# Performance work log

Hardware: AMD Instinct MI355X
Metric: run time of the kernel (lower is better)

## Reference

```python
import jax, jax.numpy as jnp
import numpy as np

B, N, V, X, H, C = 128, 1023, 32000, 256, 256, 10  # N = 2^10 - 1 perfect binary tree (heap layout)


def setup_inputs() -> dict:
    key = jax.random.key(0)
    ks = jax.random.split(key, 12)
    s = 0.02
    return {
        "wordid": jax.random.randint(ks[0], (B, N), 0, V),
        "h0": jnp.zeros((B, N, H), jnp.float32),
        "c0": jnp.zeros((B, N, H), jnp.float32),
        "emb": jax.random.normal(ks[1], (V, X), jnp.float32) * s,
        "W_iou": jax.random.normal(ks[2], (3 * H, X), jnp.float32) * s,
        "U_iou": jax.random.normal(ks[3], (3 * H, 2 * H), jnp.float32) * s,
        "b_iou": jnp.zeros((1, 3 * H), jnp.float32),
        "Uf_W": jax.random.normal(ks[4], (2 * H, 2 * H), jnp.float32) * s,
        "Uf_b": jnp.zeros((2 * H,), jnp.float32),
        "Wmem": jax.random.normal(ks[5], (H, H), jnp.float32) * s,
        "wh_W": jax.random.normal(ks[6], (H, H), jnp.float32) * s,
        "wh_b": jnp.zeros((H,), jnp.float32),
        "lin_W": jax.random.normal(ks[7], (C, H), jnp.float32) * s,
        "lin_b": jnp.zeros((C,), jnp.float32),
    }


def _apply_node(iou, b_iou, c_in):
    # TreeLSTMCell.apply_node_func: iou -> i,o,u gates; c = sig(i)*tanh(u) + c_in; h = sig(o)*tanh(c)
    i, o, u = jnp.split(iou + b_iou, 3, axis=-1)
    c = jax.nn.sigmoid(i) * jnp.tanh(u) + c_in
    h = jax.nn.sigmoid(o) * jnp.tanh(c)
    return h, c


def reference(wordid, h0, c0, emb, W_iou, U_iou, b_iou, Uf_W, Uf_b, Wmem, wh_W, wh_b, lin_W, lin_b):
    Bn, Nn, Hn = h0.shape
    D = int(np.log2(Nn + 1))  # depth of perfect binary tree
    h, c = h0, c0
    # --- leaves (frontier 0): iou = W_iou(embed), c from initial state ---
    s = 2 ** (D - 1) - 1
    x_leaf = emb[wordid[:, s:]]                                  # [B, Nleaf, X]
    iou = jnp.einsum('bnx,gx->bng', x_leaf, W_iou)               # [B, Nleaf, 3H]
    hl, cl = _apply_node(iou, b_iou, c[:, s:])
    h = h.at[:, s:].set(hl)
    c = c.at[:, s:].set(cl)
    # --- internal levels, bottom-up (reduce_func overwrites iou and c) ---
    for level in range(D - 2, -1, -1):
        ps, pe = 2 ** level - 1, 2 ** (level + 1) - 1
        npar = pe - ps
        cs, ce = pe, pe + 2 * npar  # children of parent p live at 2p+1, 2p+2 (contiguous block)
        h_cat = h[:, cs:ce].reshape(Bn, npar, 2 * Hn)            # [B, npar, 2H]
        f = jax.nn.sigmoid(jnp.einsum('bnk,jk->bnj', h_cat, Uf_W) + Uf_b)
        f = f.reshape(Bn, npar, 2, Hn)
        c_sum = jnp.sum(f * c[:, cs:ce].reshape(Bn, npar, 2, Hn), axis=2)
        iou_p = jnp.einsum('bnk,gk->bng', h_cat, U_iou)          # [B, npar, 3H]
        hp, cp = _apply_node(iou_p, b_iou, c_sum)
        h = h.at[:, ps:pe].set(hp)
        c = c.at[:, ps:pe].set(cp)
    # --- TreeAttention: root (node 0 per tree) attends over all nodes of its tree ---
    dec = h[:, 0]                                                # [B, H]
    proj = jnp.einsum('bnh,gh->bng', h, Wmem)                    # memory_project
    scores = jnp.einsum('bh,bnh->bn', dec, proj)
    attn = jax.nn.softmax(scores, axis=1)                        # MaskedSoftmax, mask=None
    context = jnp.einsum('bn,bnh->bh', attn, h)                  # [B, H]
    hid = jax.nn.relu(context @ wh_W.T + wh_b)
    return hid @ lin_W.T + lin_b                                 # [B, num_classes]
```

## Files before the change

### kernel.cpp

```cpp
#include <hip/hip_runtime.h>
#include <math.h>

#define BB      128
#define NNODES  1023
#define HD      256
#define LEAVES  512
#define IOU3    768
#define CAT2    512
#define LDCOMB  1280

typedef unsigned short ushort_t;
typedef __bf16 bf16x8 __attribute__((ext_vector_type(8)));
typedef float  f32x4  __attribute__((ext_vector_type(4)));

__device__ __forceinline__ float sigf(float x) { return 1.0f / (1.0f + expf(-x)); }

__device__ __forceinline__ void gload16(const void* g, void* l)
{
    __builtin_amdgcn_global_load_lds(
        (const __attribute__((address_space(1))) unsigned int*)g,
        (__attribute__((address_space(3))) unsigned int*)l, 16, 0, 0);
}

__device__ __forceinline__ void split_bf16(float x, ushort_t& h, ushort_t& l)
{
    unsigned u = __float_as_uint(x);
    unsigned r = u + 0x7fff + ((u >> 16) & 1);
    h = (ushort_t)(r >> 16);
    float fh = __uint_as_float((unsigned)h << 16);
    float d = x - fh;
    unsigned u2 = __float_as_uint(d);
    unsigned r2 = u2 + 0x7fff + ((u2 >> 16) & 1);
    l = (ushort_t)(r2 >> 16);
}

__device__ __forceinline__ void split4v(float4 v, ushort4& hv, ushort4& lv)
{
    split_bf16(v.x, hv.x, lv.x);
    split_bf16(v.y, hv.y, lv.y);
    split_bf16(v.z, hv.z, lv.z);
    split_bf16(v.w, hv.w, lv.w);
}

__device__ __forceinline__ float rh2(ushort_t h, ushort_t l)
{
    return __uint_as_float((unsigned)h << 16) + __uint_as_float((unsigned)l << 16);
}

__global__ void k_splits(const float* __restrict__ emb, const float* __restrict__ W_iou,
                         const float* __restrict__ Uf, const float* __restrict__ Ui,
                         ushort_t* __restrict__ ehi, ushort_t* __restrict__ elo,
                         ushort_t* __restrict__ wihi, ushort_t* __restrict__ wilo,
                         ushort_t* __restrict__ wchi, ushort_t* __restrict__ wclo,
                         int V)
{
    const int stride = gridDim.x * 256;
    const int t0 = blockIdx.x * 256 + threadIdx.x;
    ushort4 hv, lv;
    for (int i = t0; i < V * 64; i += stride) {
        split4v(((const float4*)emb)[i], hv, lv);
        ((ushort4*)ehi)[i] = hv;
        ((ushort4*)elo)[i] = lv;
    }
    for (int i = t0; i < IOU3 * 64; i += stride) {
        split4v(((const float4*)W_iou)[i], hv, lv);
        ((ushort4*)wihi)[i] = hv;
        ((ushort4*)wilo)[i] = lv;
    }
    for (int i = t0; i < 1280 * 128; i += stride) {
        int row = i >> 7, c4 = i & 127;
        const float* src = (row < 512) ? (Uf + (size_t)row * 512)
                                       : (Ui + (size_t)(row - 512) * 512);
        split4v(((const float4*)src)[c4], hv, lv);
        ((ushort4*)wchi)[i] = hv;
        ((ushort4*)wclo)[i] = lv;
    }
}

#define BM 128
#define BN 128
#define BK 32

__global__ __launch_bounds__(512, 4)
void gemm_mfma(const ushort_t* __restrict__ Ahi, const ushort_t* __restrict__ Alo,
               int lognpar, unsigned sB, int sP, int m0, int K,
               const ushort_t* __restrict__ Bhi, const ushort_t* __restrict__ Blo,
               float* __restrict__ C, int ldc)
{
    __shared__ __align__(16) char lds[65536];
    const int tid = threadIdx.x;

    int bx = blockIdx.x, by = blockIdx.y;
    {
        const int gx = gridDim.x, gy = gridDim.y;
        if ((gx & 7) == 0) {
            int f = by * gx + bx;
            int span = gy << 3;
            int s = f / span;
            int wv = f - s * span;
            bx = (s << 3) + (wv & 7);
            by = wv >> 3;
        }
    }

    const int w = tid >> 6, lane = tid & 63;

    unsigned aoff, boff;
    {
        int row = tid >> 2;
        int slotp = (tid & 3) ^ ((row >> 1) & 3);
        int mg = m0 + bx * BM + row;
        int b = mg >> lognpar;
        int q = mg & ((1 << lognpar) - 1);
        unsigned ab = (unsigned)b * sB + (unsigned)q * (unsigned)sP;
        aoff = ab + slotp * 8;
        boff = (unsigned)(by * BN + row) * (unsigned)K + slotp * 8;
    }
    const int wdst = w * 1024;

    auto STAGE = [&](int k0, char* buf) {
        gload16(Ahi + aoff + k0, buf +     0 + wdst);
        gload16(Alo + aoff + k0, buf +  8192 + wdst);
        gload16(Bhi + boff + k0, buf + 16384 + wdst);
        gload16(Blo + boff + k0, buf + 24576 + wdst);
    };

    const int wm = w >> 2, wn = w & 3;
    const int rA0 = wm * 64 + (lane & 15);
    const int rB0 = wn * 32 + (lane & 15);
    const int ko = lane >> 4;
    const int rdA = rA0 * 64 + ((ko ^ ((rA0 >> 1) & 3)) << 4);
    const int rdB = rB0 * 64 + ((ko ^ ((rB0 >> 1) & 3)) << 4);

    f32x4 acc[4][2];
#pragma unroll
    for (int mi = 0; mi < 4; ++mi)
#pragma unroll
        for (int ni = 0; ni < 2; ++ni) acc[mi][ni] = (f32x4){0.f, 0.f, 0.f, 0.f};

    const int nt = K / BK;
    STAGE(0, lds);
    int cur = 0;
    for (int t = 0; t < nt; ++t) {
        if (t + 1 < nt) {
            STAGE((t + 1) * BK, lds + (cur ^ 1) * 32768);
            asm volatile("s_waitcnt vmcnt(4)" ::: "memory");
        } else {
            asm volatile("s_waitcnt vmcnt(0)" ::: "memory");
        }
        __builtin_amdgcn_s_barrier();
        __builtin_amdgcn_sched_barrier(0);
        char* base = lds + cur * 32768;
        bf16x8 ah[4], al[4], bh[2], bl[2];
#pragma unroll
        for (int q = 0; q < 4; ++q) {
            ah[q] = *(const bf16x8*)(base +        rdA + q * 1024);
            al[q] = *(const bf16x8*)(base + 8192 + rdA + q * 1024);
        }
#pragma unroll
        for (int q = 0; q < 2; ++q) {
            bh[q] = *(const bf16x8*)(base + 16384 + rdB + q * 1024);
            bl[q] = *(const bf16x8*)(base + 24576 + rdB + q * 1024);
        }
        __builtin_amdgcn_s_setprio(1);
#pragma unroll
        for (int mi = 0; mi < 4; ++mi)
#pragma unroll
            for (int ni = 0; ni < 2; ++ni) {
                acc[mi][ni] = __builtin_amdgcn_mfma_f32_16x16x32_bf16(ah[mi], bh[ni], acc[mi][ni], 0, 0, 0);
                acc[mi][ni] = __builtin_amdgcn_mfma_f32_16x16x32_bf16(ah[mi], bl[ni], acc[mi][ni], 0, 0, 0);
                acc[mi][ni] = __builtin_amdgcn_mfma_f32_16x16x32_bf16(al[mi], bh[ni], acc[mi][ni], 0, 0, 0);
            }
        __builtin_amdgcn_s_setprio(0);
        __builtin_amdgcn_s_barrier();
        cur ^= 1;
    }

    {
        char* patch = lds + w * 2304;
        const int cl = lane & 15, rg = lane >> 4;
        const int gcol0 = by * BN + wn * 32;
#pragma unroll
        for (int mi = 0; mi < 4; ++mi) {
#pragma unroll
            for (int ni = 0; ni < 2; ++ni)
#pragma unroll
                for (int r = 0; r < 4; ++r)
                    *(float*)(patch + (rg * 4 + r) * 144 + (ni * 16 + cl) * 4) = acc[mi][ni][r];
            int grow0 = m0 + bx * BM + wm * 64 + mi * 16;
#pragma unroll
            for (int i = 0; i < 2; ++i) {
                int slot = lane + 64 * i;
                int lr = slot >> 3, c4 = slot & 7;
                f32x4 vv = *(const f32x4*)(patch + lr * 144 + c4 * 16);
                *(f32x4*)(C + (size_t)(grow0 + lr) * ldc + gcol0 + c4 * 4) = vv;
            }
        }
    }
}

__global__ void k_apply_leaf(const float* __restrict__ viou, const int* __restrict__ wordid,
                             const float* __restrict__ b_iou,
                             ushort_t* __restrict__ hhi, ushort_t* __restrict__ hlo,
                             float* __restrict__ c)
{
    int idx = blockIdx.x * 256 + threadIdx.x;
    int m_l = idx >> 8, hh = idx & 255;
    int b = m_l >> 9, leaf = m_l & 511;
    int node = 511 + leaf;
    int word = wordid[b * NNODES + node];
    const float* br = viou + (size_t)word * IOU3;
    float iv = br[hh]        + b_iou[hh];
    float ov = br[256 + hh]  + b_iou[256 + hh];
    float uv = br[512 + hh]  + b_iou[512 + hh];
    size_t nb = ((size_t)b * NNODES + node) * HD + hh;
    float cn = sigf(iv) * tanhf(uv);
    float hn = sigf(ov) * tanhf(cn);
    c[nb] = cn;
    split_bf16(hn, hhi[nb], hlo[nb]);
}

__global__ void k_apply_level(const float* __restrict__ buf, const float* __restrict__ b_iou,
                              const float* __restrict__ Uf_b,
                              ushort_t* __restrict__ hhi, ushort_t* __restrict__ hlo,
                              float* __restrict__ c,
                              int lognpar, int ps, int cs)
{
    int idx = blockIdx.x * 256 + threadIdx.x;
    int m_l = idx >> 8, hh = idx & 255;
    int b = m_l >> lognpar;
    int p = m_l & ((1 << lognpar) - 1);
    const float* br = buf + (size_t)m_l * LDCOMB;
    float fl = sigf(br[hh]        + Uf_b[hh]);
    float fr = sigf(br[256 + hh]  + Uf_b[256 + hh]);
    size_t cb = ((size_t)b * NNODES + cs + 2 * p) * HD + hh;
    float csum = fl * c[cb] + fr * c[cb + HD];
    float iv = br[512 + hh]  + b_iou[hh];
    float ov = br[768 + hh]  + b_iou[256 + hh];
    float uv = br[1024 + hh] + b_iou[512 + hh];
    float cn = sigf(iv) * tanhf(uv) + csum;
    float hn = sigf(ov) * tanhf(cn);
    size_t pb = ((size_t)b * NNODES + ps + p) * HD + hh;
    c[pb] = cn;
    split_bf16(hn, hhi[pb], hlo[pb]);
}

__global__ void k_dec_v(const ushort_t* __restrict__ hhi, const ushort_t* __restrict__ hlo,
                        const float* __restrict__ Wmem, float* __restrict__ v)
{
    int b = blockIdx.x, k = threadIdx.x;
    __shared__ float dec[HD];
    size_t base = (size_t)b * NNODES * HD;
    dec[k] = rh2(hhi[base + k], hlo[base + k]);
    __syncthreads();
    float s = 0.f;
    for (int g = 0; g < HD; ++g) s = fmaf(dec[g], Wmem[g * HD + k], s);
    v[b * HD + k] = s;
}

__global__ void k_scores(const ushort_t* __restrict__ hhi, const ushort_t* __restrict__ hlo,
                         const float* __restrict__ v, float* __restrict__ scores)
{
    int b = blockIdx.x;
    int w = threadIdx.x >> 6, lane = threadIdx.x & 63;
    int n = blockIdx.y * 4 + w;
    if (n >= NNODES) return;
    size_t hb = ((size_t)b * NNODES + n) * HD;
    ushort4 ph = *(const ushort4*)(hhi + hb + lane * 4);
    ushort4 pl = *(const ushort4*)(hlo + hb + lane * 4);
    float4 vv = *(const float4*)(v + b * HD + lane * 4);
    float s = rh2(ph.x, pl.x) * vv.x + rh2(ph.y, pl.y) * vv.y +
              rh2(ph.z, pl.z) * vv.z + rh2(ph.w, pl.w) * vv.w;
#pragma unroll
    for (int o = 32; o; o >>= 1) s += __shfl_down(s, o);
    if (lane == 0) scores[(size_t)b * NNODES + n] = s;
}

__global__ void k_context(const ushort_t* __restrict__ hhi, const ushort_t* __restrict__ hlo,
                          const float* __restrict__ scores, float* __restrict__ partial)
{
    int b = blockIdx.x, ch = blockIdx.y, k = threadIdx.x;
    __shared__ float red[4];
    __shared__ float wts[128];
    const float* srow = scores + (size_t)b * NNODES;

    float sv[4];
    float m = -INFINITY;
#pragma unroll
    for (int i = 0; i < 4; ++i) {
        int n = k + 256 * i;
        sv[i] = (n < NNODES) ? srow[n] : -INFINITY;
        m = fmaxf(m, sv[i]);
    }
#pragma unroll
    for (int o = 32; o; o >>= 1) m = fmaxf(m, __shfl_xor(m, o));
    int w = k >> 6, lane = k & 63;
    if (lane == 0) red[w] = m;
    __syncthreads();
    m = fmaxf(fmaxf(red[0], red[1]), fmaxf(red[2], red[3]));
    __syncthreads();
    float s = 0.f;
#pragma unroll
    for (int i = 0; i < 4; ++i) {
        int n = k + 256 * i;
        s += (n < NNODES) ? expf(sv[i] - m) : 0.f;
    }
#pragma unroll
    for (int o = 32; o; o >>= 1) s += __shfl_xor(s, o);
    if (lane == 0) red[w] = s;
    __syncthreads();
    float inv = 1.0f / (red[0] + red[1] + red[2] + red[3]);

    int n0 = ch * 128;
    if (k < 128) {
        int n = n0 + k;
        wts[k] = (n < NNODES) ? expf(srow[n] - m) * inv : 0.f;
    }
    __syncthreads();

    int n1 = n0 + 128; if (n1 > NNODES) n1 = NNODES;
    float acc = 0.f;
    for (int n = n0; n < n1; ++n) {
        size_t i = ((size_t)b * NNODES + n) * HD + k;
        acc = fmaf(wts[n - n0], rh2(hhi[i], hlo[i]), acc);
    }
    partial[((size_t)b * 8 + ch) * HD + k] = acc;
}

__global__ void k_final(const float* __restrict__ partial,
                        const float* __restrict__ wh_W, const float* __restrict__ wh_b,
                        const float* __restrict__ lin_W, const float* __restrict__ lin_b,
                        float* __restrict__ out)
{
    int b = blockIdx.x, j = threadIdx.x;
    __shared__ float ctx[HD];
    __shared__ float hid[HD];
    float s = 0.f;
#pragma unroll
    for (int ch = 0; ch < 8; ++ch) s += partial[((size_t)b * 8 + ch) * HD + j];
    ctx[j] = s;
    __syncthreads();
    float a = wh_b[j];
    for (int k = 0; k < HD; ++k) a = fmaf(ctx[k], wh_W[j * HD + k], a);
    hid[j] = fmaxf(a, 0.f);
    __syncthreads();
    if (j < 10) {
        float o = lin_b[j];
        for (int k = 0; k < HD; ++k) o = fmaf(hid[k], lin_W[j * HD + k], o);
        out[b * 10 + j] = o;
    }
}

extern "C" void kernel_launch(void* const* d_in, const int* in_sizes, int n_in,
                              void* d_out, int out_size, void* d_ws, size_t ws_size,
                              hipStream_t stream)
{
    const int*   wordid = (const int*)d_in[0];
    const float* emb    = (const float*)d_in[3];
    const float* W_iou  = (const float*)d_in[4];
    const float* U_iou  = (const float*)d_in[5];
    const float* b_iou  = (const float*)d_in[6];
    const float* Uf_W   = (const float*)d_in[7];
    const float* Uf_b   = (const float*)d_in[8];
    const float* Wmem   = (const float*)d_in[9];
    const float* wh_W   = (const float*)d_in[10];
    const float* wh_b   = (const float*)d_in[11];
    const float* lin_W  = (const float*)d_in[12];
    const float* lin_b  = (const float*)d_in[13];
    float* out = (float*)d_out;

    const int V = in_sizes[3] / 256;
    const size_t nh = (size_t)BB * NNODES * HD;

    char* ws = (char*)d_ws;
    size_t off = 0;
    auto alloc = [&](size_t bytes) -> void* {
        void* p = ws + off;
        off += (bytes + 255) & ~(size_t)255;
        return p;
    };
    ushort_t* hhi  = (ushort_t*)alloc(nh * 2);
    ushort_t* hlo  = (ushort_t*)alloc(nh * 2);
    float*    c    = (float*)   alloc(nh * 4);
    ushort_t* ehi  = (ushort_t*)alloc((size_t)V * 256 * 2);
    ushort_t* elo  = (ushort_t*)alloc((size_t)V * 256 * 2);
    ushort_t* wchi = (ushort_t*)alloc((size_t)LDCOMB * 512 * 2);
    ushort_t* wclo = (ushort_t*)alloc((size_t)LDCOMB * 512 * 2);
    ushort_t* wihi = (ushort_t*)alloc((size_t)IOU3 * 256 * 2);
    ushort_t* wilo = (ushort_t*)alloc((size_t)IOU3 * 256 * 2);
    float* v       = (float*)alloc((size_t)BB * HD * 4);
    float* scores  = (float*)alloc((size_t)BB * NNODES * 4);
    float* partial = (float*)alloc((size_t)BB * 8 * HD * 4);
    float* buf     = (float*)alloc((size_t)32768 * LDCOMB * 4);
    float* viou    = buf;
    (void)ws_size;

    k_splits<<<2048, 256, 0, stream>>>(emb, W_iou, Uf_W, U_iou,
                                       ehi, elo, wihi, wilo, wchi, wclo, V);

    {
        dim3 g(256, 6);
        gemm_mfma<<<g, 512, 0, stream>>>(ehi, elo, 0, 256u, 0, 0, 256,
                                         wihi, wilo, viou, IOU3);
        k_apply_leaf<<<65536, 256, 0, stream>>>(viou, wordid, b_iou, hhi, hlo, c);
    }

    for (int L = 8; L >= 0; --L) {
        int npar = 1 << L;
        int ps = npar - 1, cs = 2 * npar - 1;
        const ushort_t* Abh = hhi + (size_t)cs * HD;
        const ushort_t* Abl = hlo + (size_t)cs * HD;
        dim3 g(npar, 10);
        gemm_mfma<<<g, 512, 0, stream>>>(Abh, Abl, L,
                                         (unsigned)(NNODES * HD), 2 * HD, 0, CAT2,
                                         wchi, wclo, buf, LDCOMB);
        k_apply_level<<<BB * npar, 256, 0, stream>>>(buf, b_iou, Uf_b, hhi, hlo, c,
                                                     L, ps, cs);
    }

    k_dec_v<<<BB, HD, 0, stream>>>(hhi, hlo, Wmem, v);
    k_scores<<<dim3(BB, 256), 256, 0, stream>>>(hhi, hlo, v, scores);
    k_context<<<dim3(BB, 8), HD, 0, stream>>>(hhi, hlo, scores, partial);
    k_final<<<BB, HD, 0, stream>>>(partial, wh_W, wh_b, lin_W, lin_b, out);
}
```

Baseline: 666.9 us.

## Fuse forget-gate GEMM with per-level cell update epilogue

Splits the combined per-level GEMM into an iou GEMM that writes a narrower buffer and a new forget-gate GEMM kernel, gemm_f. gemm_f's epilogue computes the sigmoid gates, child-c sum, the cell and hidden update, and the bf16 split directly from its accumulators. Uf rows are permuted so each block's tile holds matching left and right gate columns for the same hidden indices. This removes the separate apply kernel and the write and reread of the forget-gate part of the intermediate buffer. In exchange the epilogue does scattered loads of c and ioubuf straight from global memory instead of through LDS.

```diff
diff --git a/kernel.cpp b/kernel.cpp
--- a/kernel.cpp
+++ b/kernel.cpp
@@ -7,7 +7,6 @@
 #define LEAVES  512
 #define IOU3    768
 #define CAT2    512
-#define LDCOMB  1280
 
 typedef unsigned short ushort_t;
 typedef __bf16 bf16x8 __attribute__((ext_vector_type(8)));
@@ -51,7 +50,8 @@
                          const float* __restrict__ Uf, const float* __restrict__ Ui,
                          ushort_t* __restrict__ ehi, ushort_t* __restrict__ elo,
                          ushort_t* __restrict__ wihi, ushort_t* __restrict__ wilo,
-                         ushort_t* __restrict__ wchi, ushort_t* __restrict__ wclo,
+                         ushort_t* __restrict__ uihi, ushort_t* __restrict__ uilo,
+                         ushort_t* __restrict__ wfhi, ushort_t* __restrict__ wflo,
                          int V)
 {
     const int stride = gridDim.x * 256;
@@ -67,13 +67,19 @@
         ((ushort4*)wihi)[i] = hv;
         ((ushort4*)wilo)[i] = lv;
     }
-    for (int i = t0; i < 1280 * 128; i += stride) {
-        int row = i >> 7, c4 = i & 127;
-        const float* src = (row < 512) ? (Uf + (size_t)row * 512)
-                                       : (Ui + (size_t)(row - 512) * 512);
+    for (int i = t0; i < IOU3 * 128; i += stride) {
+        split4v(((const float4*)Ui)[i], hv, lv);
+        ((ushort4*)uihi)[i] = hv;
+        ((ushort4*)uilo)[i] = lv;
+    }
+    for (int i = t0; i < 512 * 128; i += stride) {
+        int rowp = i >> 7, c4 = i & 127;
+        int hb = rowp >> 5, rem = rowp & 31;
+        int g = rem >> 4, hl = rem & 15;
+        const float* src = Uf + (size_t)(g * 256 + hb * 16 + hl) * 512;
         split4v(((const float4*)src)[c4], hv, lv);
-        ((ushort4*)wchi)[i] = hv;
-        ((ushort4*)wclo)[i] = lv;
+        ((ushort4*)wfhi)[i] = hv;
+        ((ushort4*)wflo)[i] = lv;
     }
 }
 
@@ -194,6 +200,134 @@
                 int lr = slot >> 3, c4 = slot & 7;
                 f32x4 vv = *(const f32x4*)(patch + lr * 144 + c4 * 16);
                 *(f32x4*)(C + (size_t)(grow0 + lr) * ldc + gcol0 + c4 * 4) = vv;
+            }
+        }
+    }
+}
+
+__global__ __launch_bounds__(512, 4)
+void gemm_f(const ushort_t* __restrict__ Ahi, const ushort_t* __restrict__ Alo,
+            int L, unsigned sB, int sP,
+            const ushort_t* __restrict__ Bhi, const ushort_t* __restrict__ Blo,
+            const float* __restrict__ ioubuf, const float* __restrict__ Uf_b,
+            const float* __restrict__ b_iou,
+            float* __restrict__ c, ushort_t* __restrict__ hhi, ushort_t* __restrict__ hlo,
+            int ps, int cs)
+{
+    __shared__ __align__(16) char lds[65536];
+    const int tid = threadIdx.x;
+    const int K = 512;
+
+    int bx = blockIdx.x, by = blockIdx.y;
+    {
+        const int gx = gridDim.x, gy = gridDim.y;
+        if ((gx & 7) == 0) {
+            int f = by * gx + bx;
+            int span = gy << 3;
+            int s = f / span;
+            int wv = f - s * span;
+            bx = (s << 3) + (wv & 7);
+            by = wv >> 3;
+        }
+    }
+
+    const int w = tid >> 6, lane = tid & 63;
+
+    unsigned aoff, boff;
+    {
+        int row = tid >> 2;
+        int slotp = (tid & 3) ^ ((row >> 1) & 3);
+        int mg = bx * BM + row;
+        int b = mg >> L;
+        int q = mg & ((1 << L) - 1);
+        unsigned ab = (unsigned)b * sB + (unsigned)q * (unsigned)sP;
+        aoff = ab + slotp * 8;
+        boff = (unsigned)(by * BN + row) * (unsigned)K + slotp * 8;
+    }
+    const int wdst = w * 1024;
+
+    auto STAGE = [&](int k0, char* buf) {
+        gload16(Ahi + aoff + k0, buf +     0 + wdst);
+        gload16(Alo + aoff + k0, buf +  8192 + wdst);
+        gload16(Bhi + boff + k0, buf + 16384 + wdst);
+        gload16(Blo + boff + k0, buf + 24576 + wdst);
+    };
+
+    const int wm = w >> 2, wn = w & 3;
+    const int rA0 = wm * 64 + (lane & 15);
+    const int rB0 = wn * 32 + (lane & 15);
+    const int ko = lane >> 4;
+    const int rdA = rA0 * 64 + ((ko ^ ((rA0 >> 1) & 3)) << 4);
+    const int rdB = rB0 * 64 + ((ko ^ ((rB0 >> 1) & 3)) << 4);
+
+    f32x4 acc[4][2];
+#pragma unroll
+    for (int mi = 0; mi < 4; ++mi)
+#pragma unroll
+        for (int ni = 0; ni < 2; ++ni) acc[mi][ni] = (f32x4){0.f, 0.f, 0.f, 0.f};
+
+    const int nt = K / BK;
+    STAGE(0, lds);
+    int cur = 0;
+    for (int t = 0; t < nt; ++t) {
+        if (t + 1 < nt) {
+            STAGE((t + 1) * BK, lds + (cur ^ 1) * 32768);
+            asm volatile("s_waitcnt vmcnt(4)" ::: "memory");
+        } else {
+            asm volatile("s_waitcnt vmcnt(0)" ::: "memory");
+        }
+        __builtin_amdgcn_s_barrier();
+        __builtin_amdgcn_sched_barrier(0);
+        char* base = lds + cur * 32768;
+        bf16x8 ah[4], al[4], bh[2], bl[2];
+#pragma unroll
+        for (int q = 0; q < 4; ++q) {
+            ah[q] = *(const bf16x8*)(base +        rdA + q * 1024);
+            al[q] = *(const bf16x8*)(base + 8192 + rdA + q * 1024);
+        }
+#pragma unroll
+        for (int q = 0; q < 2; ++q) {
+            bh[q] = *(const bf16x8*)(base + 16384 + rdB + q * 1024);
+            bl[q] = *(const bf16x8*)(base + 24576 + rdB + q * 1024);
+        }
+        __builtin_amdgcn_s_setprio(1);
+#pragma unroll
+        for (int mi = 0; mi < 4; ++mi)
+#pragma unroll
+            for (int ni = 0; ni < 2; ++ni) {
+                acc[mi][ni] = __builtin_amdgcn_mfma_f32_16x16x32_bf16(ah[mi], bh[ni], acc[mi][ni], 0, 0, 0);
+                acc[mi][ni] = __builtin_amdgcn_mfma_f32_16x16x32_bf16(ah[mi], bl[ni], acc[mi][ni], 0, 0, 0);
+                acc[mi][ni] = __builtin_amdgcn_mfma_f32_16x16x32_bf16(al[mi], bh[ni], acc[mi][ni], 0, 0, 0);
+            }
+        __builtin_amdgcn_s_setprio(0);
+        __builtin_amdgcn_s_barrier();
+        cur ^= 1;
+    }
+
+    {
+        const int hh = by * 64 + wn * 16 + (lane & 15);
+        const int npm1 = (1 << L) - 1;
+#pragma unroll
+        for (int mi = 0; mi < 4; ++mi) {
+            int grow0 = bx * BM + wm * 64 + mi * 16 + (lane >> 4) * 4;
+#pragma unroll
+            for (int r = 0; r < 4; ++r) {
+                int grow = grow0 + r;
+                float fl = sigf(acc[mi][0][r] + Uf_b[hh]);
+                float fr = sigf(acc[mi][1][r] + Uf_b[256 + hh]);
+                int b = grow >> L;
+                int p = grow & npm1;
+                size_t cb = ((size_t)b * NNODES + cs + 2 * p) * HD + hh;
+                float csum = fl * c[cb] + fr * c[cb + HD];
+                size_t iob = (size_t)grow * IOU3 + hh;
+                float iv = ioubuf[iob]       + b_iou[hh];
+                float ov = ioubuf[iob + 256] + b_iou[256 + hh];
+                float uv = ioubuf[iob + 512] + b_iou[512 + hh];
+                float cn = sigf(iv) * tanhf(uv) + csum;
+                float hn = sigf(ov) * tanhf(cn);
+                size_t pb = ((size_t)b * NNODES + ps + p) * HD + hh;
+                c[pb] = cn;
+                split_bf16(hn, hhi[pb], hlo[pb]);
             }
         }
     }
@@ -220,31 +354,6 @@
     split_bf16(hn, hhi[nb], hlo[nb]);
 }
 
-__global__ void k_apply_level(const float* __restrict__ buf, const float* __restrict__ b_iou,
-                              const float* __restrict__ Uf_b,
-                              ushort_t* __restrict__ hhi, ushort_t* __restrict__ hlo,
-                              float* __restrict__ c,
-                              int lognpar, int ps, int cs)
-{
-    int idx = blockIdx.x * 256 + threadIdx.x;
-    int m_l = idx >> 8, hh = idx & 255;
-    int b = m_l >> lognpar;
-    int p = m_l & ((1 << lognpar) - 1);
-    const float* br = buf + (size_t)m_l * LDCOMB;
-    float fl = sigf(br[hh]        + Uf_b[hh]);
-    float fr = sigf(br[256 + hh]  + Uf_b[256 + hh]);
-    size_t cb = ((size_t)b * NNODES + cs + 2 * p) * HD + hh;
-    float csum = fl * c[cb] + fr * c[cb + HD];
-    float iv = br[512 + hh]  + b_iou[hh];
-    float ov = br[768 + hh]  + b_iou[256 + hh];
-    float uv = br[1024 + hh] + b_iou[512 + hh];
-    float cn = sigf(iv) * tanhf(uv) + csum;
-    float hn = sigf(ov) * tanhf(cn);
-    size_t pb = ((size_t)b * NNODES + ps + p) * HD + hh;
-    c[pb] = cn;
-    split_bf16(hn, hhi[pb], hlo[pb]);
-}
-
 __global__ void k_dec_v(const ushort_t* __restrict__ hhi, const ushort_t* __restrict__ hlo,
                         const float* __restrict__ Wmem, float* __restrict__ v)
 {
@@ -384,19 +493,22 @@
     float*    c    = (float*)   alloc(nh * 4);
     ushort_t* ehi  = (ushort_t*)alloc((size_t)V * 256 * 2);
     ushort_t* elo  = (ushort_t*)alloc((size_t)V * 256 * 2);
-    ushort_t* wchi = (ushort_t*)alloc((size_t)LDCOMB * 512 * 2);
-    ushort_t* wclo = (ushort_t*)alloc((size_t)LDCOMB * 512 * 2);
     ushort_t* wihi = (ushort_t*)alloc((size_t)IOU3 * 256 * 2);
     ushort_t* wilo = (ushort_t*)alloc((size_t)IOU3 * 256 * 2);
+    ushort_t* uihi = (ushort_t*)alloc((size_t)IOU3 * 512 * 2);
+    ushort_t* uilo = (ushort_t*)alloc((size_t)IOU3 * 512 * 2);
+    ushort_t* wfhi = (ushort_t*)alloc((size_t)512 * 512 * 2);
+    ushort_t* wflo = (ushort_t*)alloc((size_t)512 * 512 * 2);
     float* v       = (float*)alloc((size_t)BB * HD * 4);
     float* scores  = (float*)alloc((size_t)BB * NNODES * 4);
     float* partial = (float*)alloc((size_t)BB * 8 * HD * 4);
-    float* buf     = (float*)alloc((size_t)32768 * LDCOMB * 4);
-    float* viou    = buf;
+    float* ioubuf  = (float*)alloc((size_t)32768 * IOU3 * 4);
+    float* viou    = ioubuf;
     (void)ws_size;
 
     k_splits<<<2048, 256, 0, stream>>>(emb, W_iou, Uf_W, U_iou,
-                                       ehi, elo, wihi, wilo, wchi, wclo, V);
+                                       ehi, elo, wihi, wilo, uihi, uilo,
+                                       wfhi, wflo, V);
 
     {
         dim3 g(256, 6);
@@ -410,12 +522,15 @@
         int ps = npar - 1, cs = 2 * npar - 1;
         const ushort_t* Abh = hhi + (size_t)cs * HD;
         const ushort_t* Abl = hlo + (size_t)cs * HD;
-        dim3 g(npar, 10);
-        gemm_mfma<<<g, 512, 0, stream>>>(Abh, Abl, L,
-                                         (unsigned)(NNODES * HD), 2 * HD, 0, CAT2,
-                                         wchi, wclo, buf, LDCOMB);
-        k_apply_level<<<BB * npar, 256, 0, stream>>>(buf, b_iou, Uf_b, hhi, hlo, c,
-                                                     L, ps, cs);
+        dim3 g1(npar, 6);
+        gemm_mfma<<<g1, 512, 0, stream>>>(Abh, Abl, L,
+                                          (unsigned)(NNODES * HD), 2 * HD, 0, CAT2,
+                                          uihi, uilo, ioubuf, IOU3);
+        dim3 g2(npar, 4);
+        gemm_f<<<g2, 512, 0, stream>>>(Abh, Abl, L,
+                                       (unsigned)(NNODES * HD), 2 * HD,
+                                       wfhi, wflo, ioubuf, Uf_b, b_iou,
+                                       c, hhi, hlo, ps, cs);
     }
 
     k_dec_v<<<BB, HD, 0, stream>>>(hhi, hlo, Wmem, v);
```

Measured after the change: 756.7 us. +13.5%, slower.
